# Kernel tuning notes

Measured on AMD Instinct MI355X. Metric: run time of the kernel, lower is better.

## Reference

```python
import jax, jax.numpy as jnp
from jax import lax
import numpy as np

B, T, V = 2048, 128, 25
H = 512          # num_hidden
NUM_CLASSES = 100


def setup_inputs() -> dict:
    key = jax.random.key(0)
    ks = jax.random.split(key, 7)
    messages = jax.random.normal(ks[0], (B, T, V), dtype=jnp.float32)
    # LSTMCell params (PyTorch layout: weight_ih [4H, V], weight_hh [4H, H], gate order i,f,g,o)
    W_ih = jax.random.normal(ks[1], (4 * H, V), dtype=jnp.float32) * (1.0 / np.sqrt(V))
    W_hh = jax.random.normal(ks[2], (4 * H, H), dtype=jnp.float32) * (1.0 / np.sqrt(H))
    b_ih = jnp.zeros((4 * H,), dtype=jnp.float32)
    # forget-gate bias initialized to 1 (as in initialize_parameters)
    b_hh = jnp.zeros((4 * H,), dtype=jnp.float32).at[H:2 * H].set(1.0)
    W_fc = jax.random.normal(ks[3], (NUM_CLASSES, H), dtype=jnp.float32) * (1.0 / np.sqrt(H))
    b_fc = jnp.zeros((NUM_CLASSES,), dtype=jnp.float32)
    return {"messages": messages, "W_ih": W_ih, "W_hh": W_hh,
            "b_ih": b_ih, "b_hh": b_hh, "W_fc": W_fc, "b_fc": b_fc}


def reference(messages, W_ih, W_hh, b_ih, b_hh, W_fc, b_fc):
    b, t, v = messages.shape
    h_dim = W_hh.shape[1]
    # Batch the input-to-hidden projection across all timesteps up front: [B,T,4H]
    x_proj = jnp.einsum('btv,gv->btg', messages, W_ih) + b_ih + b_hh
    xs = jnp.swapaxes(x_proj, 0, 1)  # [T, B, 4H] for scan over time

    def step(carry, x_g):
        h, c = carry
        gates = x_g + h @ W_hh.T                       # [B, 4H]
        i, f, g, o = jnp.split(gates, 4, axis=-1)      # PyTorch gate order i,f,g,o
        i = jax.nn.sigmoid(i)
        f = jax.nn.sigmoid(f)
        g = jnp.tanh(g)
        o = jax.nn.sigmoid(o)
        c = f * c + i * g
        h = o * jnp.tanh(c)
        return (h, c), None

    init = (jnp.zeros((b, h_dim), dtype=messages.dtype),
            jnp.zeros((b, h_dim), dtype=messages.dtype))
    (h_last, _), _ = lax.scan(step, init, xs)
    return h_last @ W_fc.T + b_fc  # [B, num_classes]
```

## Files before the change

kernel.cpp:

```cpp
#include <hip/hip_runtime.h>

#define BB 2048
#define TT 128
#define VV 25
#define HH 512
#define NC 100

typedef __attribute__((ext_vector_type(8))) _Float16 half8;
typedef __attribute__((ext_vector_type(4))) float f32x4;

__device__ __forceinline__ float fsigmoid(float x) { return 1.0f / (1.0f + __expf(-x)); }
__device__ __forceinline__ float ftanh(float x) {
    float e = __expf(2.0f * x);
    return 1.0f - 2.0f / (e + 1.0f);
}

__global__ __launch_bounds__(256) void prep_whh_t(const float* __restrict__ W,
                                                  _Float16* __restrict__ WT) {
    int i = blockIdx.x * 256 + threadIdx.x;
    int n = i & 2047, kq = i >> 11;
    half8 h8;
    #pragma unroll
    for (int j = 0; j < 8; ++j) h8[j] = (_Float16)W[(size_t)n * HH + kq * 8 + j];
    ((half8*)WT)[(size_t)kq * 2048 + n] = h8;
}

__global__ __launch_bounds__(256) void prep_wih_t(const float* __restrict__ W,
                                                  _Float16* __restrict__ WT) {
    int i = blockIdx.x * 256 + threadIdx.x;
    int n = i & 2047, kq4 = i >> 11;
    half8 h8;
    #pragma unroll
    for (int j = 0; j < 8; ++j) {
        int k = kq4 * 8 + j;
        h8[j] = (k < VV) ? (_Float16)W[(size_t)n * VV + k] : (_Float16)0.0f;
    }
    ((half8*)WT)[(size_t)(64 + kq4) * 2048 + n] = h8;
}

__global__ __launch_bounds__(256, 2) void lstm_step(
    const float* __restrict__ msg, int t,
    const _Float16* __restrict__ WT,
    const float* __restrict__ b_ih, const float* __restrict__ b_hh,
    const _Float16* __restrict__ hin, _Float16* __restrict__ hout,
    float* __restrict__ c)
{
    const int b0 = blockIdx.x * 64;
    const int j0 = blockIdx.y * 32;
    const int tid = threadIdx.x;
    const int lane = tid & 63;
    const int w = tid >> 6;
    const int wm = w & 1, wn = w >> 1;
    const int col = lane & 15, quad = lane >> 4;
    const int jj = j0 + wn * 16 + col;

    __shared__ _Float16 Abuf[2][64][72];

    f32x4 acc[2][4];
    #pragma unroll
    for (int g = 0; g < 4; ++g) {
        float bias = b_ih[g * HH + jj] + b_hh[g * HH + jj];
        f32x4 bv = {bias, bias, bias, bias};
        acc[0][g] = bv;
        acc[1][g] = bv;
    }

    const int arow = tid >> 2, aseg = (tid & 3) << 4;
    const _Float16* aph = hin + (size_t)(b0 + arow) * HH + aseg;

    const half8* WT8 = (const half8*)WT;
    int bidx[4];
    #pragma unroll
    for (int g = 0; g < 4; ++g) bidx[g] = quad * 2048 + g * HH + j0 + wn * 16 + col;

    half8 Bs[2][4];
    half8 ra[2];

    ra[0] = *(const half8*)(aph);
    ra[1] = *(const half8*)(aph + 8);
    #pragma unroll
    for (int g = 0; g < 4; ++g) Bs[0][g] = WT8[bidx[g]];
    *(half8*)&Abuf[0][arow][aseg]     = ra[0];
    *(half8*)&Abuf[0][arow][aseg + 8] = ra[1];
    ra[0] = *(const half8*)(aph + 64);
    ra[1] = *(const half8*)(aph + 72);
    #pragma unroll
    for (int g = 0; g < 4; ++g) Bs[1][g] = WT8[8192 + bidx[g]];
    __syncthreads();

    float xv[8];
    const int xseg = (tid & 3) << 3;

    for (int it = 0; it < 8; ++it) {
        const int buf = it & 1;
        #pragma unroll
        for (int kk = 0; kk < 2; ++kk) {
            const int cchunk = it * 2 + kk;
            const int p = cchunk & 1;
            half8 ahf[2];
            #pragma unroll
            for (int tm = 0; tm < 2; ++tm)
                ahf[tm] = *(const half8*)&Abuf[buf][wm * 32 + tm * 16 + col][kk * 32 + quad * 8];
            #pragma unroll
            for (int tm = 0; tm < 2; ++tm)
                #pragma unroll
                for (int g = 0; g < 4; ++g)
                    acc[tm][g] = __builtin_amdgcn_mfma_f32_16x16x32_f16(ahf[tm], Bs[p][g], acc[tm][g], 0, 0, 0);
            if (cchunk + 2 <= 16) {
                const int ix = (cchunk + 2) * 8192;
                #pragma unroll
                for (int g = 0; g < 4; ++g) Bs[p][g] = WT8[ix + bidx[g]];
            }
        }
        if (it < 7) {
            *(half8*)&Abuf[buf ^ 1][arow][aseg]     = ra[0];
            *(half8*)&Abuf[buf ^ 1][arow][aseg + 8] = ra[1];
            if (it < 6) {
                const int kt = (it + 2) * 64;
                ra[0] = *(const half8*)(aph + kt);
                ra[1] = *(const half8*)(aph + kt + 8);
            } else {
                const size_t mb = ((size_t)(b0 + arow) * TT + t) * VV;
                #pragma unroll
                for (int i = 0; i < 8; ++i) {
                    int k = xseg + i;
                    xv[i] = (k < VV) ? msg[mb + k] : 0.0f;
                }
            }
        } else {
            half8 xh;
            #pragma unroll
            for (int i = 0; i < 8; ++i) xh[i] = (_Float16)xv[i];
            *(half8*)&Abuf[0][arow][xseg] = xh;
        }
        __syncthreads();
    }

    {
        half8 ahf[2];
        #pragma unroll
        for (int tm = 0; tm < 2; ++tm)
            ahf[tm] = *(const half8*)&Abuf[0][wm * 32 + tm * 16 + col][quad * 8];
        #pragma unroll
        for (int tm = 0; tm < 2; ++tm)
            #pragma unroll
            for (int g = 0; g < 4; ++g)
                acc[tm][g] = __builtin_amdgcn_mfma_f32_16x16x32_f16(ahf[tm], Bs[0][g], acc[tm][g], 0, 0, 0);
    }

    #pragma unroll
    for (int tm = 0; tm < 2; ++tm) {
        #pragma unroll
        for (int reg = 0; reg < 4; ++reg) {
            int b = b0 + wm * 32 + tm * 16 + quad * 4 + reg;
            size_t idx = (size_t)b * HH + jj;
            float i_ = fsigmoid(acc[tm][0][reg]);
            float f_ = fsigmoid(acc[tm][1][reg]);
            float g_ = ftanh(acc[tm][2][reg]);
            float o_ = fsigmoid(acc[tm][3][reg]);
            float cn = f_ * c[idx] + i_ * g_;
            c[idx] = cn;
            hout[idx] = (_Float16)(o_ * ftanh(cn));
        }
    }
}

__global__ __launch_bounds__(256) void fc_kernel(
    const _Float16* __restrict__ h, const float* __restrict__ W_fc,
    const float* __restrict__ b_fc, float* __restrict__ out)
{
    __shared__ float hs[4][HH];
    const int b0 = blockIdx.x * 4;
    for (int i = threadIdx.x; i < 4 * HH; i += 256) {
        int r = i >> 9, k = i & 511;
        hs[r][k] = (float)h[(size_t)(b0 + r) * HH + k];
    }
    __syncthreads();
    const int tid = threadIdx.x;
    if (tid < 2 * NC) {
        int r = tid / NC, cls = tid % NC;
        const float4* wv = (const float4*)(W_fc + (size_t)cls * HH);
        const float4* h0 = (const float4*)hs[r];
        const float4* h1 = (const float4*)hs[r + 2];
        float s0 = 0.0f, s1 = 0.0f;
        #pragma unroll 4
        for (int k = 0; k < HH / 4; ++k) {
            float4 ww = wv[k];
            float4 a0 = h0[k], a1 = h1[k];
            s0 += a0.x * ww.x + a0.y * ww.y + a0.z * ww.z + a0.w * ww.w;
            s1 += a1.x * ww.x + a1.y * ww.y + a1.z * ww.z + a1.w * ww.w;
        }
        out[(size_t)(b0 + r) * NC + cls] = s0 + b_fc[cls];
        out[(size_t)(b0 + r + 2) * NC + cls] = s1 + b_fc[cls];
    }
}

extern "C" void kernel_launch(void* const* d_in, const int* in_sizes, int n_in,
                              void* d_out, int out_size, void* d_ws, size_t ws_size,
                              hipStream_t stream) {
    const float* msg  = (const float*)d_in[0];
    const float* W_ih = (const float*)d_in[1];
    const float* W_hh = (const float*)d_in[2];
    const float* b_ih = (const float*)d_in[3];
    const float* b_hh = (const float*)d_in[4];
    const float* W_fc = (const float*)d_in[5];
    const float* b_fc = (const float*)d_in[6];
    float* out = (float*)d_out;

    float*    c  = (float*)d_ws;
    _Float16* h0 = (_Float16*)(c + (size_t)BB * HH);
    _Float16* h1 = h0 + (size_t)BB * HH;
    _Float16* WT = h1 + (size_t)BB * HH;

    hipMemsetAsync(d_ws, 0, (size_t)BB * HH * 4 + (size_t)BB * HH * 2, stream);

    prep_whh_t<<<512, 256, 0, stream>>>(W_hh, WT);
    prep_wih_t<<<32, 256, 0, stream>>>(W_ih, WT);

    _Float16 *hin = h0, *hout = h1;
    for (int t = 0; t < TT; ++t) {
        lstm_step<<<dim3(BB / 64, HH / 32), 256, 0, stream>>>(
            msg, t, WT, b_ih, b_hh, hin, hout, c);
        _Float16* tmp = hin; hin = hout; hout = tmp;
    }
    fc_kernel<<<BB / 4, 256, 0, stream>>>(hin, W_fc, b_fc, out);
}
```

Measured before the change: 1.564 ms.

## Load LSTM A operands directly from global into registers with 4-deep prefetch

Removes the shared-memory staging of the hidden state and the per-iteration __syncthreads, so each lane loads its MFMA A fragments straight from global memory into registers. A 4-stage register ring prefetches both A and B fragments four chunks ahead across a fully unrolled 17-chunk K loop, with the message input folded in as the last chunk. This drops barrier and LDS traffic, but A rows are now read redundantly by the two wn warps, and the larger register footprint may reduce occupancy.

```diff
diff --git a/kernel.cpp b/kernel.cpp
--- a/kernel.cpp
+++ b/kernel.cpp
@@ -54,8 +54,6 @@
     const int col = lane & 15, quad = lane >> 4;
     const int jj = j0 + wn * 16 + col;
 
-    __shared__ _Float16 Abuf[2][64][72];
-
     f32x4 acc[2][4];
     #pragma unroll
     for (int g = 0; g < 4; ++g) {
@@ -65,87 +63,54 @@
         acc[1][g] = bv;
     }
 
-    const int arow = tid >> 2, aseg = (tid & 3) << 4;
-    const _Float16* aph = hin + (size_t)(b0 + arow) * HH + aseg;
+    const _Float16* arow[2];
+    #pragma unroll
+    for (int tm = 0; tm < 2; ++tm)
+        arow[tm] = hin + (size_t)(b0 + wm * 32 + tm * 16 + col) * HH + quad * 8;
 
     const half8* WT8 = (const half8*)WT;
     int bidx[4];
     #pragma unroll
     for (int g = 0; g < 4; ++g) bidx[g] = quad * 2048 + g * HH + j0 + wn * 16 + col;
 
-    half8 Bs[2][4];
-    half8 ra[2];
-
-    ra[0] = *(const half8*)(aph);
-    ra[1] = *(const half8*)(aph + 8);
+    half8 As[4][2], Bs[4][4];
     #pragma unroll
-    for (int g = 0; g < 4; ++g) Bs[0][g] = WT8[bidx[g]];
-    *(half8*)&Abuf[0][arow][aseg]     = ra[0];
-    *(half8*)&Abuf[0][arow][aseg + 8] = ra[1];
-    ra[0] = *(const half8*)(aph + 64);
-    ra[1] = *(const half8*)(aph + 72);
-    #pragma unroll
-    for (int g = 0; g < 4; ++g) Bs[1][g] = WT8[8192 + bidx[g]];
-    __syncthreads();
-
-    float xv[8];
-    const int xseg = (tid & 3) << 3;
-
-    for (int it = 0; it < 8; ++it) {
-        const int buf = it & 1;
+    for (int p = 0; p < 4; ++p) {
         #pragma unroll
-        for (int kk = 0; kk < 2; ++kk) {
-            const int cchunk = it * 2 + kk;
-            const int p = cchunk & 1;
-            half8 ahf[2];
-            #pragma unroll
-            for (int tm = 0; tm < 2; ++tm)
-                ahf[tm] = *(const half8*)&Abuf[buf][wm * 32 + tm * 16 + col][kk * 32 + quad * 8];
-            #pragma unroll
-            for (int tm = 0; tm < 2; ++tm)
-                #pragma unroll
-                for (int g = 0; g < 4; ++g)
-                    acc[tm][g] = __builtin_amdgcn_mfma_f32_16x16x32_f16(ahf[tm], Bs[p][g], acc[tm][g], 0, 0, 0);
-            if (cchunk + 2 <= 16) {
-                const int ix = (cchunk + 2) * 8192;
-                #pragma unroll
-                for (int g = 0; g < 4; ++g) Bs[p][g] = WT8[ix + bidx[g]];
-            }
-        }
-        if (it < 7) {
-            *(half8*)&Abuf[buf ^ 1][arow][aseg]     = ra[0];
-            *(half8*)&Abuf[buf ^ 1][arow][aseg + 8] = ra[1];
-            if (it < 6) {
-                const int kt = (it + 2) * 64;
-                ra[0] = *(const half8*)(aph + kt);
-                ra[1] = *(const half8*)(aph + kt + 8);
-            } else {
-                const size_t mb = ((size_t)(b0 + arow) * TT + t) * VV;
-                #pragma unroll
-                for (int i = 0; i < 8; ++i) {
-                    int k = xseg + i;
-                    xv[i] = (k < VV) ? msg[mb + k] : 0.0f;
-                }
-            }
-        } else {
-            half8 xh;
-            #pragma unroll
-            for (int i = 0; i < 8; ++i) xh[i] = (_Float16)xv[i];
-            *(half8*)&Abuf[0][arow][xseg] = xh;
-        }
-        __syncthreads();
+        for (int tm = 0; tm < 2; ++tm) As[p][tm] = *(const half8*)(arow[tm] + p * 32);
+        #pragma unroll
+        for (int g = 0; g < 4; ++g) Bs[p][g] = WT8[p * 8192 + bidx[g]];
     }
 
-    {
-        half8 ahf[2];
-        #pragma unroll
-        for (int tm = 0; tm < 2; ++tm)
-            ahf[tm] = *(const half8*)&Abuf[0][wm * 32 + tm * 16 + col][quad * 8];
+    #pragma unroll
+    for (int cc = 0; cc < 17; ++cc) {
+        const int s = cc & 3;
         #pragma unroll
         for (int tm = 0; tm < 2; ++tm)
             #pragma unroll
             for (int g = 0; g < 4; ++g)
-                acc[tm][g] = __builtin_amdgcn_mfma_f32_16x16x32_f16(ahf[tm], Bs[0][g], acc[tm][g], 0, 0, 0);
+                acc[tm][g] = __builtin_amdgcn_mfma_f32_16x16x32_f16(As[s][tm], Bs[s][g], acc[tm][g], 0, 0, 0);
+        const int nc = cc + 4;
+        if (nc <= 15) {
+            #pragma unroll
+            for (int tm = 0; tm < 2; ++tm) As[s][tm] = *(const half8*)(arow[tm] + nc * 32);
+            #pragma unroll
+            for (int g = 0; g < 4; ++g) Bs[s][g] = WT8[nc * 8192 + bidx[g]];
+        } else if (nc == 16) {
+            #pragma unroll
+            for (int tm = 0; tm < 2; ++tm) {
+                const float* mrow = msg + ((size_t)(b0 + wm * 32 + tm * 16 + col) * TT + t) * VV;
+                half8 xh;
+                #pragma unroll
+                for (int i = 0; i < 8; ++i) {
+                    int k = quad * 8 + i;
+                    xh[i] = (k < VV) ? (_Float16)mrow[k] : (_Float16)0.0f;
+                }
+                As[s][tm] = xh;
+            }
+            #pragma unroll
+            for (int g = 0; g < 4; ++g) Bs[s][g] = WT8[16 * 8192 + bidx[g]];
+        }
     }
 
     #pragma unroll
```

Result: slower. 2.559 ms (+63.6%).
